# Optimization experiments

Measured on AMD Instinct MI355X. Metric: run time of the kernel, lower is better.

The kernel has to match this reference:

```python
import jax, jax.numpy as jnp
import numpy as np

M, N, D = 8192, 8192, 256
GAMMA = 1.0 / D  # RBF bandwidth


def setup_inputs() -> dict:
    key = jax.random.key(0)
    k1, k2, k3 = jax.random.split(key, 3)
    Xq = jax.random.normal(k1, (M, D), dtype=jnp.float32)
    Xtrain = jax.random.normal(k2, (N, D), dtype=jnp.float32)
    alpha = jax.random.normal(k3, (N, 1), dtype=jnp.float32)
    return {"Xq": Xq, "Xtrain": Xtrain, "alpha": alpha}


def rbf_kernel(A, B):
    # squared euclidean distances via ||a||^2 + ||b||^2 - 2 a.b  -> [M, N]
    sq_a = jnp.sum(A * A, axis=1, keepdims=True)          # [M,1]
    sq_b = jnp.sum(B * B, axis=1, keepdims=True).T        # [1,N]
    d2 = sq_a + sq_b - 2.0 * jnp.einsum('md,nd->mn', A, B)
    d2 = jnp.maximum(d2, 0.0)
    return jnp.exp(-GAMMA * d2)


def reference(Xq, Xtrain, alpha):
    # forward: kernel(X, self.X) @ self.alpha  -> [M, 1]
    K = rbf_kernel(Xq, Xtrain)
    return K @ alpha
```

## Files before the change

kernel.cpp:

```cpp
#include <hip/hip_runtime.h>
#include <stdint.h>


#define MM 8192
#define NN 8192
#define DD 256
#define GAMMA (1.0f/256.0f)
#define LOG2E 1.44269504088896340736f
#define SCALE_A (2.0f*GAMMA*LOG2E)
#define NEG_G_LOG2E (-GAMMA*LOG2E)

#define NSPLIT 16
#define NPB (NN/NSPLIT)
#define NT_PER (NPB/16)

typedef __bf16 bf16x8 __attribute__((ext_vector_type(8)));
typedef float  f32x4  __attribute__((ext_vector_type(4)));

#define A_OFF  ((size_t)0)
#define B_OFF  ((size_t)4 << 20)
#define W_OFF  ((size_t)8 << 20)
#define EA_OFF (((size_t)8 << 20) + 32768)
#define PART_OFF (((size_t)8 << 20) + 65536)

__device__ __forceinline__ unsigned short f2bf(float f) {
  union { float f; uint32_t u; } x; x.f = f;
  uint32_t u = x.u;
  u += 0x7FFFu + ((u >> 16) & 1u);
  return (unsigned short)(u >> 16);
}
__device__ __forceinline__ uint32_t pack2(float a, float b) {
  return (uint32_t)f2bf(a) | ((uint32_t)f2bf(b) << 16);
}

__global__ __launch_bounds__(256) void prep_kernel(
    const float* __restrict__ Xq, const float* __restrict__ Xt,
    const float* __restrict__ alpha,
    char* __restrict__ Amat, char* __restrict__ Bmat,
    float* __restrict__ w, float* __restrict__ ea)
{
  const int lane = threadIdx.x & 63;
  const int gw = blockIdx.x * 4 + (threadIdx.x >> 6);
  const bool isA = gw < 512;
  const int t = isA ? gw : gw - 512;
  const float* __restrict__ src = isA ? Xq : Xt;
  char* __restrict__ dst = isA ? Amat : Bmat;
  const float sc = isA ? SCALE_A : 1.0f;
  const int n = t * 16 + (lane & 15);
  float ss = 0.f;
#pragma unroll
  for (int r = 0; r < 8; ++r) {
    const int gg = r * 4 + (lane >> 4);
    const float* p = src + (size_t)n * DD + gg * 8;
    const float4 f0 = *(const float4*)p;
    const float4 f1 = *(const float4*)(p + 4);
    ss += f0.x*f0.x + f0.y*f0.y + f0.z*f0.z + f0.w*f0.w
        + f1.x*f1.x + f1.y*f1.y + f1.z*f1.z + f1.w*f1.w;
    uint4 pk;
    pk.x = pack2(f0.x * sc, f0.y * sc); pk.y = pack2(f0.z * sc, f0.w * sc);
    pk.z = pack2(f1.x * sc, f1.y * sc); pk.w = pack2(f1.z * sc, f1.w * sc);
    *(uint4*)(dst + (size_t)t * 8192 + r * 1024 + lane * 16) = pk;
  }
  ss += __shfl_xor(ss, 16, 64);
  ss += __shfl_xor(ss, 32, 64);
  if (lane < 16) {
    if (isA) ea[n] = __builtin_amdgcn_exp2f(NEG_G_LOG2E * ss);
    else     w[n]  = alpha[n] * __builtin_amdgcn_exp2f(NEG_G_LOG2E * ss);
  }
}

__global__ __launch_bounds__(256, 3) void rbf_main(
    const char* __restrict__ Amat, const char* __restrict__ Bmat,
    const float* __restrict__ w, const float* __restrict__ ea,
    float* __restrict__ part)
{
  const int tid  = threadIdx.x;
  const int wave = tid >> 6, lane = tid & 63;
  const int quad = lane >> 4, l16 = lane & 15;

  const int b    = blockIdx.x;
  const int xcd  = b & 7, slot = b >> 3;
  const int my   = (xcd & 3) * 16 + (slot & 15);
  const int nx   = (xcd >> 2) * 8 + (slot >> 4);
  const int mt0    = my * 8 + wave * 2;
  const int nt0    = nx * NT_PER;
  const int nbase0 = nx * NPB;

  bf16x8 afrag[2][8];
#pragma unroll
  for (int rt = 0; rt < 2; ++rt)
#pragma unroll
    for (int kc = 0; kc < 8; ++kc) {
      union { uint4 u; bf16x8 v; } cv;
      cv.u = *(const uint4*)(Amat + (size_t)(mt0 + rt) * 8192 + kc * 1024 + lane * 16);
      afrag[rt][kc] = cv.v;
    }

  const f32x4 fzero = {0.f, 0.f, 0.f, 0.f};
  float outacc[2][4] = {{0.f,0.f,0.f,0.f},{0.f,0.f,0.f,0.f}};

  for (int ct = 0; ct < NT_PER; ++ct) {
    union { uint4 u; bf16x8 v; } bf[8];
#pragma unroll
    for (int kc = 0; kc < 8; ++kc)
      bf[kc].u = *(const uint4*)(Bmat + (size_t)(nt0 + ct) * 8192 + kc * 1024 + lane * 16);
    const float wv = w[nbase0 + ct * 16 + l16];
    f32x4 acc[2][2] = {{fzero, fzero}, {fzero, fzero}};
#pragma unroll
    for (int kc = 0; kc < 8; ++kc) {
      acc[0][kc & 1] = __builtin_amdgcn_mfma_f32_16x16x32_bf16(afrag[0][kc], bf[kc].v, acc[0][kc & 1], 0, 0, 0);
      acc[1][kc & 1] = __builtin_amdgcn_mfma_f32_16x16x32_bf16(afrag[1][kc], bf[kc].v, acc[1][kc & 1], 0, 0, 0);
    }
#pragma unroll
    for (int rt = 0; rt < 2; ++rt) {
      const f32x4 s = acc[rt][0] + acc[rt][1];
      outacc[rt][0] += wv * __builtin_amdgcn_exp2f(s[0]);
      outacc[rt][1] += wv * __builtin_amdgcn_exp2f(s[1]);
      outacc[rt][2] += wv * __builtin_amdgcn_exp2f(s[2]);
      outacc[rt][3] += wv * __builtin_amdgcn_exp2f(s[3]);
    }
  }

#pragma unroll
  for (int rt = 0; rt < 2; ++rt)
#pragma unroll
    for (int i = 0; i < 4; ++i) {
      float v = outacc[rt][i];
      v += __shfl_xor(v, 1, 64);
      v += __shfl_xor(v, 2, 64);
      v += __shfl_xor(v, 4, 64);
      v += __shfl_xor(v, 8, 64);
      if (l16 == 0) {
        const int row = my * 128 + wave * 32 + rt * 16 + quad * 4 + i;
        part[(size_t)nx * MM + row] = ea[row] * v;
      }
    }
}

__global__ __launch_bounds__(256) void reduce_kernel(
    const float* __restrict__ part, float* __restrict__ out)
{
  const int row = blockIdx.x * 256 + threadIdx.x;
  float s = 0.f;
#pragma unroll
  for (int i = 0; i < NSPLIT; ++i) s += part[(size_t)i * MM + row];
  out[row] = s;
}

extern "C" void kernel_launch(void* const* d_in, const int* in_sizes, int n_in,
                              void* d_out, int out_size, void* d_ws, size_t ws_size,
                              hipStream_t stream) {
  const float* Xq    = (const float*)d_in[0];
  const float* Xt    = (const float*)d_in[1];
  const float* alpha = (const float*)d_in[2];
  float* out = (float*)d_out;
  char*  ws  = (char*)d_ws;

  char*  Amat = ws + A_OFF;
  char*  Bmat = ws + B_OFF;
  float* w    = (float*)(ws + W_OFF);
  float* ea   = (float*)(ws + EA_OFF);
  float* part = (float*)(ws + PART_OFF);

  hipLaunchKernelGGL(prep_kernel, dim3(256), dim3(256), 0, stream,
                     Xq, Xt, alpha, Amat, Bmat, w, ea);
  hipLaunchKernelGGL(rbf_main, dim3(NSPLIT * 64), dim3(256), 0, stream,
                     Amat, Bmat, w, ea, part);
  hipLaunchKernelGGL(reduce_kernel, dim3(MM / 256), dim3(256), 0, stream,
                     part, out);
}
```

Before: 108.5 us.

## Double per-wave row tiles and double-buffer B fragment loads in RBF kernel

Each wave now holds four 16-row A tiles instead of two, so every B fragment loaded from global memory feeds four MFMAs. This halves B traffic per unit of compute, and the grid shrinks to 512 blocks. B loads are also software-pipelined with two register buffers so the next tile's loads are in flight while the current one computes. The cost is more VGPRs (occupancy hint lowered from 3 to 2 blocks) and only 512 blocks on a 256-CU device, which may leave latency less hidden. Each MFMA chain now uses one accumulator instead of two interleaved ones.

```diff
diff --git a/kernel.cpp b/kernel.cpp
--- a/kernel.cpp
+++ b/kernel.cpp
@@ -69,7 +69,7 @@
   }
 }
 
-__global__ __launch_bounds__(256, 3) void rbf_main(
+__global__ __launch_bounds__(256, 2) void rbf_main(
     const char* __restrict__ Amat, const char* __restrict__ Bmat,
     const float* __restrict__ w, const float* __restrict__ ea,
     float* __restrict__ part)
@@ -80,15 +80,15 @@
 
   const int b    = blockIdx.x;
   const int xcd  = b & 7, slot = b >> 3;
-  const int my   = (xcd & 3) * 16 + (slot & 15);
-  const int nx   = (xcd >> 2) * 8 + (slot >> 4);
-  const int mt0    = my * 8 + wave * 2;
+  const int my   = (xcd & 3) * 8 + (slot & 7);
+  const int nx   = (xcd >> 2) * 8 + (slot >> 3);
+  const int mt0    = my * 16 + wave * 4;
   const int nt0    = nx * NT_PER;
   const int nbase0 = nx * NPB;
 
-  bf16x8 afrag[2][8];
+  bf16x8 afrag[4][8];
 #pragma unroll
-  for (int rt = 0; rt < 2; ++rt)
+  for (int rt = 0; rt < 4; ++rt)
 #pragma unroll
     for (int kc = 0; kc < 8; ++kc) {
       union { uint4 u; bf16x8 v; } cv;
@@ -96,33 +96,45 @@
       afrag[rt][kc] = cv.v;
     }
 
-  const f32x4 fzero = {0.f, 0.f, 0.f, 0.f};
-  float outacc[2][4] = {{0.f,0.f,0.f,0.f},{0.f,0.f,0.f,0.f}};
+  float outacc[4][4] = {{0,0,0,0},{0,0,0,0},{0,0,0,0},{0,0,0,0}};
 
-  for (int ct = 0; ct < NT_PER; ++ct) {
-    union { uint4 u; bf16x8 v; } bf[8];
+  uint4 bufA[8], bufB[8];
+  auto loadB = [&](uint4* dst, int ct) {
 #pragma unroll
     for (int kc = 0; kc < 8; ++kc)
-      bf[kc].u = *(const uint4*)(Bmat + (size_t)(nt0 + ct) * 8192 + kc * 1024 + lane * 16);
+      dst[kc] = *(const uint4*)(Bmat + (size_t)(nt0 + ct) * 8192 + kc * 1024 + lane * 16);
+  };
+
+  const f32x4 fzero = {0.f, 0.f, 0.f, 0.f};
+  auto compute = [&](const uint4* buf, int ct) {
     const float wv = w[nbase0 + ct * 16 + l16];
-    f32x4 acc[2][2] = {{fzero, fzero}, {fzero, fzero}};
+    f32x4 acc[4] = {fzero, fzero, fzero, fzero};
 #pragma unroll
     for (int kc = 0; kc < 8; ++kc) {
-      acc[0][kc & 1] = __builtin_amdgcn_mfma_f32_16x16x32_bf16(afrag[0][kc], bf[kc].v, acc[0][kc & 1], 0, 0, 0);
-      acc[1][kc & 1] = __builtin_amdgcn_mfma_f32_16x16x32_bf16(afrag[1][kc], bf[kc].v, acc[1][kc & 1], 0, 0, 0);
+      union { uint4 u; bf16x8 v; } cv; cv.u = buf[kc];
+#pragma unroll
+      for (int rt = 0; rt < 4; ++rt)
+        acc[rt] = __builtin_amdgcn_mfma_f32_16x16x32_bf16(afrag[rt][kc], cv.v, acc[rt], 0, 0, 0);
     }
 #pragma unroll
-    for (int rt = 0; rt < 2; ++rt) {
-      const f32x4 s = acc[rt][0] + acc[rt][1];
-      outacc[rt][0] += wv * __builtin_amdgcn_exp2f(s[0]);
-      outacc[rt][1] += wv * __builtin_amdgcn_exp2f(s[1]);
-      outacc[rt][2] += wv * __builtin_amdgcn_exp2f(s[2]);
-      outacc[rt][3] += wv * __builtin_amdgcn_exp2f(s[3]);
+    for (int rt = 0; rt < 4; ++rt) {
+      outacc[rt][0] += wv * __builtin_amdgcn_exp2f(acc[rt][0]);
+      outacc[rt][1] += wv * __builtin_amdgcn_exp2f(acc[rt][1]);
+      outacc[rt][2] += wv * __builtin_amdgcn_exp2f(acc[rt][2]);
+      outacc[rt][3] += wv * __builtin_amdgcn_exp2f(acc[rt][3]);
     }
+  };
+
+  loadB(bufA, 0);
+  for (int ct = 0; ct < NT_PER; ct += 2) {
+    loadB(bufB, ct + 1);
+    compute(bufA, ct);
+    if (ct + 2 < NT_PER) loadB(bufA, ct + 2);
+    compute(bufB, ct + 1);
   }
 
 #pragma unroll
-  for (int rt = 0; rt < 2; ++rt)
+  for (int rt = 0; rt < 4; ++rt)
 #pragma unroll
     for (int i = 0; i < 4; ++i) {
       float v = outacc[rt][i];
@@ -131,7 +143,7 @@
       v += __shfl_xor(v, 4, 64);
       v += __shfl_xor(v, 8, 64);
       if (l16 == 0) {
-        const int row = my * 128 + wave * 32 + rt * 16 + quad * 4 + i;
+        const int row = my * 256 + wave * 64 + rt * 16 + quad * 4 + i;
         part[(size_t)nx * MM + row] = ea[row] * v;
       }
     }
@@ -164,7 +176,7 @@
 
   hipLaunchKernelGGL(prep_kernel, dim3(256), dim3(256), 0, stream,
                      Xq, Xt, alpha, Amat, Bmat, w, ea);
-  hipLaunchKernelGGL(rbf_main, dim3(NSPLIT * 64), dim3(256), 0, stream,
+  hipLaunchKernelGGL(rbf_main, dim3(512), dim3(256), 0, stream,
                      Amat, Bmat, w, ea, part);
   hipLaunchKernelGGL(reduce_kernel, dim3(MM / 256), dim3(256), 0, stream,
                      part, out);
```

Result: faster. 102.1 us (-5.9%).
